# Kernel optimization log

Hardware: AMD Instinct MI355X
Metric: run time of the kernel (lower is better)

Reference implementation:

```python
import jax, jax.numpy as jnp
import numpy as np

L, B, D_IN, D_OUT, K = 2048, 16, 512, 512, 3  # K=3 -> prev=1, after=1 taps for both directions


def setup_inputs() -> dict:
    key = jax.random.key(0)
    ks = jax.random.split(key, 6)
    scale = 1.0 / np.sqrt(D_IN)
    return {
        "input": jax.random.normal(ks[0], (L, B, D_IN), dtype=jnp.float32),
        "lengths": jnp.full((B,), L, dtype=jnp.int32),  # unused by forward body (faithful)
        "fwd_W": jax.random.normal(ks[1], (K, D_IN, 3 * D_OUT), dtype=jnp.float32) * scale,
        "fwd_b": jax.random.normal(ks[2], (K, 3 * D_OUT), dtype=jnp.float32) * scale,
        "rev_W": jax.random.normal(ks[3], (K, D_IN, 3 * D_OUT), dtype=jnp.float32) * scale,
        "rev_b": jax.random.normal(ks[4], (K, 3 * D_OUT), dtype=jnp.float32) * scale,
    }


def _gates(x, W, b):
    # x: [L,B,D_in], W: [K,D_in,3*D_out], b: [K,3*D_out]
    y = jnp.einsum('lbd,kde->klbe', x, W) + b[:, None, None, :]
    out = y[1]  # center tap (previous_size == 1)
    # previous tap: output[1:] += y0[:-1]
    out = out + jnp.concatenate([jnp.zeros_like(y[0][:1]), y[0][:-1]], axis=0)
    # after tap: output[:-1] += y2[1:]
    out = out + jnp.concatenate([y[2][1:], jnp.zeros_like(y[2][:1])], axis=0)
    f, o, z = jnp.split(out, 3, axis=-1)
    return jax.nn.sigmoid(f), jax.nn.sigmoid(o), jnp.tanh(z)


def _pool(f, o, z, init_cell, reverse=False):
    # cell_t = f_t * z_t + (1 - f_t) * cell_{t-1}  (fo-pool linear recurrence)
    def step(c, ft_fzt):
        ft, fzt = ft_fzt
        c = fzt + (1.0 - ft) * c
        return c, c
    _, cells = jax.lax.scan(step, init_cell, (f, f * z), reverse=reverse)
    return cells * o, cells  # lax.scan(reverse=True) stacks in original time order


def reference(input, lengths, fwd_W, fwd_b, rev_W, rev_b):
    init_cell = jnp.zeros((input.shape[1], D_OUT), dtype=input.dtype)
    f, o, z = _gates(input, fwd_W, fwd_b)
    hidden, cell = _pool(f, o, z, init_cell, reverse=False)
    fr, orr, zr = _gates(input, rev_W, rev_b)
    rhidden, rcell = _pool(fr, orr, zr, init_cell, reverse=True)
    output = jnp.concatenate([hidden, rhidden], axis=-1)          # [L,B,2*D_out]
    last_hidden = jnp.concatenate([hidden[-1], rhidden[-1]], -1)  # torch code uses [-1] for both
    last_cell = jnp.concatenate([cell[-1], rcell[-1]], -1)
    return output, last_hidden, last_cell
```

## Files before the change

kernel.cpp:

```cpp
#include <hip/hip_runtime.h>

#define L_SEQ 2048
#define BATCH 16
#define DIN   512
#define NOUT  1536
#define GSTRIDE 3072
#define MROWS (L_SEQ*BATCH)
#define PROWS ((L_SEQ+2)*BATCH)
#define NTILES 48

typedef float    f32x4 __attribute__((ext_vector_type(4)));
typedef float    f32x2 __attribute__((ext_vector_type(2)));
typedef _Float16 half8 __attribute__((ext_vector_type(8)));
typedef _Float16 half2v __attribute__((ext_vector_type(2)));

static __device__ __forceinline__ float sigm(float x) { return 1.f / (1.f + __expf(-x)); }
static __device__ __forceinline__ float tanh_f(float x) {
  float ax = fabsf(x);
  float t = __expf(-2.f * ax);
  float r = (1.f - t) / (1.f + t);
  return x < 0.f ? -r : r;
}

__global__ __launch_bounds__(256) void prep_x(const float* __restrict__ x,
                                              _Float16* __restrict__ xh) {
  int gid = blockIdx.x * 256 + threadIdx.x;
  int pr = gid >> 6, seg = gid & 63;
  int l = (pr >> 4) - 1;
  half8 h = (half8)0;
  if (l >= 0 && l < L_SEQ) {
    const float* src = x + (size_t)(pr - 16) * DIN + seg * 8;
#pragma unroll
    for (int i = 0; i < 8; ++i) h[i] = (_Float16)src[i];
  }
  *(half8*)(xh + (size_t)gid * 8) = h;
}

__global__ __launch_bounds__(256) void prep_w(const float* __restrict__ Wf, const float* __restrict__ Wr,
                                              _Float16* __restrict__ wTf, _Float16* __restrict__ wTr) {
  __shared__ float tile[32][33];
  int bid = blockIdx.x;
  int dir = bid & 1; bid >>= 1;
  int et = bid % 48; bid /= 48;
  int dt = bid % 16; int k = bid / 16;
  const float* W = dir ? Wr : Wf;
  _Float16* th = dir ? wTr : wTf;
  int tx = threadIdx.x & 31, ty = threadIdx.x >> 5;
  int d0 = dt * 32, e0 = et * 32;
  const float* Wk = W + (size_t)k * DIN * NOUT;
#pragma unroll
  for (int r = 0; r < 4; ++r)
    tile[ty + r * 8][tx] = Wk[(size_t)(d0 + ty + r * 8) * NOUT + e0 + tx];
  __syncthreads();
#pragma unroll
  for (int r = 0; r < 4; ++r) {
    int e = e0 + ty + r * 8;
    size_t o = (size_t)k * NOUT * DIN + (size_t)e * DIN + d0 + tx;
    th[o] = (_Float16)tile[tx][ty + r * 8];
  }
}

static __device__ __forceinline__ void gload16(const void* g, void* l) {
  __builtin_amdgcn_global_load_lds((const __attribute__((address_space(1))) void*)g,
                                   (__attribute__((address_space(3))) void*)l, 16, 0, 0);
}

__global__ __launch_bounds__(256, 2) void gemm_gates(
    const _Float16* __restrict__ xh,
    const _Float16* __restrict__ wTf,
    const _Float16* __restrict__ wTr,
    const float* __restrict__ biasf,
    const float* __restrict__ biasr,
    _Float16* __restrict__ g)
{
  __shared__ _Float16 AB[24576];
  const int tid = threadIdx.x;
  const int wave = tid >> 6, lane = tid & 63;
  int bid = blockIdx.x;
  const int xcd = bid & 7, t0 = bid >> 3;
  const int mt = xcd * 16 + t0 / 24, nt = t0 % 24;
  const int dir = nt / 12, ntd = nt % 12;
  const int brow = mt * 256, bcol = ntd * 128;

  const _Float16* wTh = dir ? wTr : wTf;
  const float* bias   = dir ? biasr : biasf;

  const int aw_col = ((tid & 3) ^ ((tid >> 3) & 3)) * 8;

  const _Float16* xbase = xh + (size_t)brow * DIN;
  const _Float16* wbase = wTh + (size_t)bcol * DIN;

  f32x4 acc[8][4];
#pragma unroll
  for (int i = 0; i < 8; ++i)
#pragma unroll
    for (int j = 0; j < 4; ++j) acc[i][j] = (f32x4)(0.f);

  const int wm = (wave >> 1) * 128, wn = (wave & 1) * 64;
  const int fr = lane & 15;
  const int fko = (((lane >> 4) ^ ((fr >> 1) & 3))) * 8;

  auto stage = [&](int t, int buf) {
    int k = t >> 4, kk = (t & 15) * 32;
    const _Float16* xs = xbase + (size_t)(16 * k) * DIN + kk + aw_col;
    const _Float16* ws = wbase + (size_t)k * NOUT * DIN + kk + aw_col;
#pragma unroll
    for (int c = 0; c < 4; ++c) {
      int row = c * 64 + (tid >> 2);
      gload16(xs + (size_t)row * DIN, AB + buf * 8192 + (c * 64 + (wave * 16)) * 32);
    }
#pragma unroll
    for (int c = 0; c < 2; ++c) {
      int row = c * 64 + (tid >> 2);
      gload16(ws + (size_t)row * DIN, AB + 16384 + buf * 4096 + (c * 64 + (wave * 16)) * 32);
    }
  };

  stage(0, 0);
  for (int t = 0; t < NTILES; ++t) {
    int buf = t & 1;
    if (t + 1 < NTILES) {
      stage(t + 1, buf ^ 1);
      asm volatile("s_waitcnt vmcnt(6)" ::: "memory");
    } else {
      asm volatile("s_waitcnt vmcnt(0)" ::: "memory");
    }
    __builtin_amdgcn_s_barrier();
    __builtin_amdgcn_sched_barrier(0);
    const _Float16* la = AB + buf * 8192;
    const _Float16* lb = AB + 16384 + buf * 4096;
    half8 a[8], b[4];
#pragma unroll
    for (int i = 0; i < 8; ++i)
      a[i] = *(const half8*)(la + (wm + i * 16 + fr) * 32 + fko);
#pragma unroll
    for (int j = 0; j < 4; ++j)
      b[j] = *(const half8*)(lb + (wn + j * 16 + fr) * 32 + fko);
    __builtin_amdgcn_s_setprio(1);
#pragma unroll
    for (int i = 0; i < 8; ++i)
#pragma unroll
      for (int j = 0; j < 4; ++j)
        acc[i][j] = __builtin_amdgcn_mfma_f32_16x16x32_f16(a[i], b[j], acc[i][j], 0, 0, 0);
    __builtin_amdgcn_s_setprio(0);
    __builtin_amdgcn_sched_barrier(0);
    __builtin_amdgcn_s_barrier();
  }

  const float* b0 = bias;
  const float* b1 = bias + NOUT;
  const float* b2 = bias + 2 * NOUT;
#pragma unroll
  for (int j = 0; j < 4; ++j) {
    int col = bcol + wn + j * 16 + fr;
    float bb0 = b0[col], bb1 = b1[col], bb2 = b2[col];
    size_t gcol = (size_t)dir * NOUT + col;
#pragma unroll
    for (int i = 0; i < 8; ++i) {
#pragma unroll
      for (int q = 0; q < 4; ++q) {
        int grow = brow + wm + i * 16 + (lane >> 4) * 4 + q;
        int l = grow >> 4;
        float bs = bb1 + (l > 0 ? bb0 : 0.f) + (l < L_SEQ - 1 ? bb2 : 0.f);
        g[(size_t)grow * GSTRIDE + gcol] = (_Float16)(acc[i][j][q] + bs);
      }
    }
  }
}

__global__ __launch_bounds__(256) void pool_phase1(const _Float16* __restrict__ g,
                                                   float* __restrict__ Aarr, float* __restrict__ Bvarr) {
  int gid = blockIdx.x * 256 + threadIdx.x;
  int rev = gid >> 17;
  int idx = gid & 131071;
  int q = idx >> 12, sidx = idx & 4095;
  int b = sidx >> 8, j = (sidx & 255) * 2;
  const _Float16* gf = g + (size_t)b * GSTRIDE + (size_t)rev * NOUT + j;
  float A0 = 1.f, Bv0 = 0.f, A1 = 1.f, Bv1 = 0.f;
  int l0 = q * 64;
#pragma unroll 4
  for (int t = 0; t < 64; ++t) {
    int l = rev ? (l0 + 63 - t) : (l0 + t);
    size_t off = (size_t)l * (BATCH * GSTRIDE);
    half2v fp = *(const half2v*)(gf + off);
    half2v zp = *(const half2v*)(gf + off + 1024);
    float f0 = sigm((float)fp[0]), f1 = sigm((float)fp[1]);
    float z0 = tanh_f((float)zp[0]), z1 = tanh_f((float)zp[1]);
    Bv0 = f0 * z0 + (1.f - f0) * Bv0;  A0 *= (1.f - f0);
    Bv1 = f1 * z1 + (1.f - f1) * Bv1;  A1 *= (1.f - f1);
  }
  size_t o = (size_t)rev * 262144 + (size_t)q * 8192 + (size_t)b * 512 + j;
  *(f32x2*)(Aarr + o) = f32x2{A0, A1};
  *(f32x2*)(Bvarr + o) = f32x2{Bv0, Bv1};
}

__global__ __launch_bounds__(256) void pool_phase3(const _Float16* __restrict__ g,
                                                   const float* __restrict__ Aarr,
                                                   const float* __restrict__ Bvarr,
                                                   float* __restrict__ out,
                                                   float* __restrict__ lh, float* __restrict__ lc) {
  int gid = blockIdx.x * 256 + threadIdx.x;
  int rev = gid >> 17;
  int idx = gid & 131071;
  int q = idx >> 12, sidx = idx & 4095;
  int b = sidx >> 8, j = (sidx & 255) * 2;
  const _Float16* gf = g + (size_t)b * GSTRIDE + (size_t)rev * NOUT + j;
  const float* Ad = Aarr + (size_t)rev * 262144;
  const float* Bd = Bvarr + (size_t)rev * 262144;
  size_t so = (size_t)b * 512 + j;
  float c0 = 0.f, c1 = 0.f;
  if (!rev) {
    for (int s = 0; s < q; ++s) {
      size_t o = (size_t)s * 8192 + so;
      f32x2 Ap = *(const f32x2*)(Ad + o);
      f32x2 Bp = *(const f32x2*)(Bd + o);
      c0 = Ap[0] * c0 + Bp[0];
      c1 = Ap[1] * c1 + Bp[1];
    }
  } else {
    for (int s = 31; s > q; --s) {
      size_t o = (size_t)s * 8192 + so;
      f32x2 Ap = *(const f32x2*)(Ad + o);
      f32x2 Bp = *(const f32x2*)(Bd + o);
      c0 = Ap[0] * c0 + Bp[0];
      c1 = Ap[1] * c1 + Bp[1];
    }
  }
  int l0 = q * 64;
#pragma unroll 2
  for (int t = 0; t < 64; ++t) {
    int l = rev ? (l0 + 63 - t) : (l0 + t);
    size_t off = (size_t)l * (BATCH * GSTRIDE);
    half2v fp = *(const half2v*)(gf + off);
    half2v op = *(const half2v*)(gf + off + 512);
    half2v zp = *(const half2v*)(gf + off + 1024);
    float f0 = sigm((float)fp[0]), f1 = sigm((float)fp[1]);
    float o0 = sigm((float)op[0]), o1 = sigm((float)op[1]);
    float z0 = tanh_f((float)zp[0]), z1 = tanh_f((float)zp[1]);
    c0 = f0 * z0 + (1.f - f0) * c0;
    c1 = f1 * z1 + (1.f - f1) * c1;
    float h0 = c0 * o0, h1 = c1 * o1;
    *(f32x2*)(out + (size_t)(l * BATCH + b) * 1024 + rev * 512 + j) = f32x2{h0, h1};
    if (l == L_SEQ - 1) {
      *(f32x2*)(lh + b * 1024 + rev * 512 + j) = f32x2{h0, h1};
      *(f32x2*)(lc + b * 1024 + rev * 512 + j) = f32x2{c0, c1};
    }
  }
}

extern "C" void kernel_launch(void* const* d_in, const int* in_sizes, int n_in,
                              void* d_out, int out_size, void* d_ws, size_t ws_size,
                              hipStream_t stream) {
  const float* x    = (const float*)d_in[0];
  const float* fwdW = (const float*)d_in[2];
  const float* fwdb = (const float*)d_in[3];
  const float* revW = (const float*)d_in[4];
  const float* revb = (const float*)d_in[5];

  float* out = (float*)d_out;
  float* lh  = out + (size_t)L_SEQ * BATCH * 1024;
  float* lc  = lh + BATCH * 1024;

  char* ws = (char*)d_ws;
  size_t off = 0;
  _Float16* g = (_Float16*)(ws + off);        off += (size_t)MROWS * GSTRIDE * 2;
  _Float16* xhp = (_Float16*)(ws + off);      off += (size_t)PROWS * DIN * 2;
  _Float16* wTf = (_Float16*)(ws + off);      off += (size_t)3 * NOUT * DIN * 2;
  _Float16* wTr = (_Float16*)(ws + off);      off += (size_t)3 * NOUT * DIN * 2;
  float* Aarr  = (float*)(ws + off); off += (size_t)2 * 32 * 8192 * 4;
  float* Bvarr = (float*)(ws + off); off += (size_t)2 * 32 * 8192 * 4;

  prep_x<<<8200, 256, 0, stream>>>(x, xhp);
  prep_w<<<4608, 256, 0, stream>>>(fwdW, revW, wTf, wTr);

  gemm_gates<<<3072, 256, 0, stream>>>(xhp, wTf, wTr, fwdb, revb, g);
  pool_phase1<<<1024, 256, 0, stream>>>(g, Aarr, Bvarr);
  pool_phase3<<<1024, 256, 0, stream>>>(g, Aarr, Bvarr, out, lh, lc);
}
```

Baseline: 468.2 us.

## Triple-buffer GEMM LDS tiles and split each K-step into two interleaved halves

The gates GEMM moves from double to triple buffering in LDS, prefetching two tiles ahead. Each K-step is split into two MFMA halves, with global-to-LDS loads for tile t+2 issued between them and A fragments loaded per half. This is meant to hide global load latency and overlap LDS reads with MFMA work. In exchange it uses more LDS (72KB per block), which may limit occupancy at 2 blocks per CU, and adds extra barriers per iteration.

```diff
diff --git a/kernel.cpp b/kernel.cpp
--- a/kernel.cpp
+++ b/kernel.cpp
@@ -73,7 +73,7 @@
     const float* __restrict__ biasr,
     _Float16* __restrict__ g)
 {
-  __shared__ _Float16 AB[24576];
+  __shared__ _Float16 AB[36864];
   const int tid = threadIdx.x;
   const int wave = tid >> 6, lane = tid & 63;
   int bid = blockIdx.x;
@@ -100,50 +100,78 @@
   const int fr = lane & 15;
   const int fko = (((lane >> 4) ^ ((fr >> 1) & 3))) * 8;
 
-  auto stage = [&](int t, int buf) {
-    int k = t >> 4, kk = (t & 15) * 32;
+  auto stage_a = [&](int t, int c) {
+    int k = t >> 4, kk = (t & 15) * 32, buf = t % 3;
     const _Float16* xs = xbase + (size_t)(16 * k) * DIN + kk + aw_col;
+    gload16(xs + (size_t)(c * 64 + (tid >> 2)) * DIN,
+            AB + buf * 8192 + (c * 64 + (wave * 16)) * 32);
+  };
+  auto stage_b = [&](int t, int c) {
+    int k = t >> 4, kk = (t & 15) * 32, buf = t % 3;
     const _Float16* ws = wbase + (size_t)k * NOUT * DIN + kk + aw_col;
-#pragma unroll
-    for (int c = 0; c < 4; ++c) {
-      int row = c * 64 + (tid >> 2);
-      gload16(xs + (size_t)row * DIN, AB + buf * 8192 + (c * 64 + (wave * 16)) * 32);
-    }
-#pragma unroll
-    for (int c = 0; c < 2; ++c) {
-      int row = c * 64 + (tid >> 2);
-      gload16(ws + (size_t)row * DIN, AB + 16384 + buf * 4096 + (c * 64 + (wave * 16)) * 32);
-    }
+    gload16(ws + (size_t)(c * 64 + (tid >> 2)) * DIN,
+            AB + 24576 + buf * 4096 + (c * 64 + (wave * 16)) * 32);
   };
-
-  stage(0, 0);
+  auto stage_all = [&](int t) {
+#pragma unroll
+    for (int c = 0; c < 4; ++c) stage_a(t, c);
+#pragma unroll
+    for (int c = 0; c < 2; ++c) stage_b(t, c);
+  };
+
+  stage_all(0);
+  stage_all(1);
+  asm volatile("s_waitcnt vmcnt(6)" ::: "memory");
+  __builtin_amdgcn_s_barrier();
+
+  half8 a[4], b[4];
   for (int t = 0; t < NTILES; ++t) {
-    int buf = t & 1;
-    if (t + 1 < NTILES) {
-      stage(t + 1, buf ^ 1);
+    const int buf = t % 3;
+    const _Float16* la = AB + buf * 8192;
+    const _Float16* lb = AB + 24576 + buf * 4096;
+
+    if (t + 2 < NTILES) { stage_a(t + 2, 0); stage_a(t + 2, 1); stage_b(t + 2, 0); }
+#pragma unroll
+    for (int i = 0; i < 4; ++i)
+      a[i] = *(const half8*)(la + (wm + i * 16 + fr) * 32 + fko);
+#pragma unroll
+    for (int j = 0; j < 4; ++j)
+      b[j] = *(const half8*)(lb + (wn + j * 16 + fr) * 32 + fko);
+    __builtin_amdgcn_sched_barrier(0);
+    __builtin_amdgcn_s_barrier();
+    asm volatile("s_waitcnt lgkmcnt(0)" ::: "memory");
+    __builtin_amdgcn_sched_barrier(0);
+    __builtin_amdgcn_s_setprio(1);
+#pragma unroll
+    for (int i = 0; i < 4; ++i)
+#pragma unroll
+      for (int j = 0; j < 4; ++j)
+        acc[i][j] = __builtin_amdgcn_mfma_f32_16x16x32_f16(a[i], b[j], acc[i][j], 0, 0, 0);
+    __builtin_amdgcn_s_setprio(0);
+    __builtin_amdgcn_sched_barrier(0);
+    __builtin_amdgcn_s_barrier();
+
+    if (t + 2 < NTILES) { stage_a(t + 2, 2); stage_a(t + 2, 3); stage_b(t + 2, 1); }
+#pragma unroll
+    for (int i = 0; i < 4; ++i)
+      a[i] = *(const half8*)(la + (wm + 64 + i * 16 + fr) * 32 + fko);
+    __builtin_amdgcn_sched_barrier(0);
+    __builtin_amdgcn_s_barrier();
+    asm volatile("s_waitcnt lgkmcnt(0)" ::: "memory");
+    __builtin_amdgcn_sched_barrier(0);
+    __builtin_amdgcn_s_setprio(1);
+#pragma unroll
+    for (int i = 0; i < 4; ++i)
+#pragma unroll
+      for (int j = 0; j < 4; ++j)
+        acc[i + 4][j] = __builtin_amdgcn_mfma_f32_16x16x32_f16(a[i], b[j], acc[i + 4][j], 0, 0, 0);
+    __builtin_amdgcn_s_setprio(0);
+    __builtin_amdgcn_sched_barrier(0);
+    if (t + 2 < NTILES) {
       asm volatile("s_waitcnt vmcnt(6)" ::: "memory");
     } else {
       asm volatile("s_waitcnt vmcnt(0)" ::: "memory");
     }
-    __builtin_amdgcn_s_barrier();
-    __builtin_amdgcn_sched_barrier(0);
-    const _Float16* la = AB + buf * 8192;
-    const _Float16* lb = AB + 16384 + buf * 4096;
-    half8 a[8], b[4];
-#pragma unroll
-    for (int i = 0; i < 8; ++i)
-      a[i] = *(const half8*)(la + (wm + i * 16 + fr) * 32 + fko);
-#pragma unroll
-    for (int j = 0; j < 4; ++j)
-      b[j] = *(const half8*)(lb + (wn + j * 16 + fr) * 32 + fko);
-    __builtin_amdgcn_s_setprio(1);
-#pragma unroll
-    for (int i = 0; i < 8; ++i)
-#pragma unroll
-      for (int j = 0; j < 4; ++j)
-        acc[i][j] = __builtin_amdgcn_mfma_f32_16x16x32_f16(a[i], b[j], acc[i][j], 0, 0, 0);
-    __builtin_amdgcn_s_setprio(0);
-    __builtin_amdgcn_sched_barrier(0);
     __builtin_amdgcn_s_barrier();
   }
 
```

Measured after the change: 473.3 us. About the same (+1.1%).
